# Kernel tuning notes

Hardware: AMD Instinct MI355X
Metric: run time of the kernel (lower is better)

## Reference

```python
import jax, jax.numpy as jnp
import numpy as np

B, T_MEL, CIN = 1, 128, 80
H = 16                      # n_height
N_FLOW, N_LAYER = 8, 8
RES = 128                   # residual = gate = skip = filter_size
IN_CH = 1
T = T_MEL * 256
SQRT_HALF = 0.7071067811865476
DIL_H = [2 ** (i % 3) for i in range(N_LAYER)]
DIL_W = [2 ** i for i in range(N_LAYER)]


def conv1x1(x, w, b):
    # x: [B,C,H,W], w: [O,C], b: [O]
    return jnp.einsum('oc,bchw->bohw', w, x) + b[None, :, None, None]


def causal_conv(x, w, b, dh, dw):
    # 3x3 conv, causal over height (pad top 2*dh), same over width
    out = jax.lax.conv_general_dilated(x, w, (1, 1), ((2 * dh, 0), (dw, dw)),
                                       rhs_dilation=(dh, dw),
                                       dimension_numbers=('NCHW', 'OIHW', 'NCHW'))
    return out + b[None, :, None, None]


def conv_transpose_1ch(x, w, b):
    # torch ConvTranspose2d(1,1,(3,32),padding=(1,8),stride=(1,16)) as dilated conv
    wf = w[::-1, ::-1][None, None]  # flipped kernel [1,1,3,32]
    out = jax.lax.conv_general_dilated(x, wf, (1, 1), ((1, 1), (23, 23)),
                                       lhs_dilation=(1, 16),
                                       dimension_numbers=('NCHW', 'OIHW', 'NCHW'))
    return out + b


def leaky(x):
    return jnp.where(x > 0, x, 0.4 * x)  # LeakyReLU(0.4)


def upsample(c, uw1, ub1, uw2, ub2):
    c = c[:, None]  # [B,1,CIN,T_mel]
    c = leaky(conv_transpose_1ch(c, uw1, ub1))
    c = leaky(conv_transpose_1ch(c, uw2, ub2))
    return c[:, 0]  # [B,CIN,256*T_mel]


def squeeze2d(a, h):
    # [B,C,T] -> [B,C,h,T//h] with adjacent samples along height
    b_, c_, t_ = a.shape
    return a.reshape(b_, c_, t_ // h, h).transpose(0, 1, 3, 2)


def wavenet(x, c, fw, fb, fgw, fgb, fgcw, fgcb, rsw, rsb):
    h = conv1x1(x, fw, fb)  # front 1x1 conv -> RES channels
    skip = 0.0
    for l in range(N_LAYER):
        hg = causal_conv(h, fgw[l], fgb[l], DIL_H[l], DIL_W[l]) + conv1x1(c, fgcw[l], fgcb[l])
        out = jnp.tanh(hg[:, :RES]) * jax.nn.sigmoid(hg[:, RES:])
        h = (h + conv1x1(out, rsw[l], rsb[l])) * SQRT_HALF
        skip = skip + out
    return skip


def waveflow_forward(x, c, front_w, front_b, fg_w, fg_b, fgc_w, fgc_b, rs_w, rs_b,
                     proj_w, proj_b, proj_scale, up_w1, up_b1, up_w2, up_b2):
    c_up = upsample(c, up_w1, up_b1, up_w2, up_b2)[:, :, :T]
    out = squeeze2d(x[:, None], H)   # [B,1,H,W]
    c2 = squeeze2d(c_up, H)          # [B,CIN,H,W]
    logdet = jnp.asarray(0.0, x.dtype)
    for i in range(N_FLOW):
        feat = wavenet(out[:, :, :-1], c2[:, :, 1:],
                       front_w[i], front_b[i], fg_w[i], fg_b[i],
                       fgc_w[i], fgc_b[i], rs_w[i], rs_b[i])
        # ZeroConv2d: 1x1 conv then * exp(3*scale)
        ls_t = conv1x1(feat, proj_w[i], proj_b[i]) * jnp.exp(proj_scale[i] * 3.0)[None, :, None, None]
        log_s, t = ls_t[:, :IN_CH], ls_t[:, IN_CH:]
        x_new = out[:, :, 1:] * jnp.exp(log_s) + t
        out = jnp.concatenate([out[:, :, :1], x_new], axis=2)
        logdet = logdet + jnp.sum(log_s)
        out = out[:, :, ::-1]   # reverse_order over height after every flow
        c2 = c2[:, :, ::-1]
    return out, logdet


def setup_inputs():
    key = jax.random.key(0)
    ks = jax.random.split(key, 10)
    inp = {
        'x': jax.random.normal(ks[0], (B, T), jnp.float32),
        'c': jax.random.normal(ks[1], (B, CIN, T_MEL), jnp.float32),
        'front_w': jax.random.normal(ks[2], (N_FLOW, RES, IN_CH), jnp.float32) * 0.05,
        'front_b': jnp.zeros((N_FLOW, RES), jnp.float32),
        'fg_w': jax.random.normal(ks[3], (N_FLOW, N_LAYER, 2 * RES, RES, 3, 3), jnp.float32) * 0.02,
        'fg_b': jnp.zeros((N_FLOW, N_LAYER, 2 * RES), jnp.float32),
        'fgc_w': jax.random.normal(ks[4], (N_FLOW, N_LAYER, 2 * RES, CIN), jnp.float32) * 0.05,
        'fgc_b': jnp.zeros((N_FLOW, N_LAYER, 2 * RES), jnp.float32),
        'rs_w': jax.random.normal(ks[5], (N_FLOW, N_LAYER, RES, RES), jnp.float32) * 0.05,
        'rs_b': jnp.zeros((N_FLOW, N_LAYER, RES), jnp.float32),
        'proj_w': jax.random.normal(ks[6], (N_FLOW, 2 * IN_CH, RES), jnp.float32) * 0.01,
        'proj_b': jnp.zeros((N_FLOW, 2 * IN_CH), jnp.float32),
        'proj_scale': jnp.zeros((N_FLOW, 2 * IN_CH), jnp.float32),
        'up_w1': jax.random.normal(ks[7], (3, 32), jnp.float32) * 0.1,
        'up_b1': jnp.zeros((), jnp.float32),
        'up_w2': jax.random.normal(ks[8], (3, 32), jnp.float32) * 0.1,
        'up_b2': jnp.zeros((), jnp.float32),
    }
    return inp


def reference(x, c, front_w, front_b, fg_w, fg_b, fgc_w, fgc_b, rs_w, rs_b,
              proj_w, proj_b, proj_scale, up_w1, up_b1, up_w2, up_b2):
    return waveflow_forward(x, c, front_w, front_b, fg_w, fg_b, fgc_w, fgc_b,
                            rs_w, rs_b, proj_w, proj_b, proj_scale,
                            up_w1, up_b1, up_w2, up_b2)
```

## Files before the change

### kernel.cpp

```cpp
#include <hip/hip_runtime.h>
#include <math.h>

#define SQH 0.70710678118654752f
typedef unsigned short u16;
using bf16x8 = __attribute__((ext_vector_type(8))) short;
using f32x4  = __attribute__((ext_vector_type(4))) float;

__device__ __forceinline__ u16 bfhi(float v) {
    unsigned u = __builtin_bit_cast(unsigned, v);
    return (u16)((u + 0x7FFFu + ((u >> 16) & 1u)) >> 16);
}
__device__ __forceinline__ float bf2f(u16 h) {
    unsigned u = ((unsigned)h) << 16;
    return __builtin_bit_cast(float, u);
}
__device__ __forceinline__ void split2(float v, u16& hi, u16& lo) {
    hi = bfhi(v);
    lo = bfhi(v - bf2f(hi));
}
__device__ __forceinline__ void gl_lds16(const void* g, void* l) {
    __builtin_amdgcn_global_load_lds(
        (const __attribute__((address_space(1))) unsigned*)g,
        (__attribute__((address_space(3))) unsigned*)l, 16, 0, 0);
}

__global__ void upsample_k(const float* __restrict__ in, int Tin,
                           const float* __restrict__ w, const float* __restrict__ bb,
                           float* __restrict__ out, int Tout)
{
    int idx = blockIdx.x * 256 + threadIdx.x;
    if (idx >= 80 * Tout) return;
    int oh = idx / Tout, ow = idx - oh * Tout;
    float acc = bb[0];
    int kw0 = (23 - (ow & 15)) & 15;
#pragma unroll
    for (int kh = 0; kh < 3; ++kh) {
        int ih = oh - 1 + kh;
        if (ih < 0 || ih >= 80) continue;
#pragma unroll
        for (int m = 0; m < 2; ++m) {
            int kw = kw0 + 16 * m;
            int j = ow - 23 + kw;
            if (j < 0) continue;
            int src = j >> 4;
            if (src < Tin)
                acc = fmaf(w[(2 - kh) * 32 + (31 - kw)], in[ih * Tin + src], acc);
        }
    }
    out[idx] = acc > 0.f ? acc : 0.4f * acc;
}

__global__ void squeeze_x_k(const float* __restrict__ x, float* __restrict__ o)
{
    int idx = blockIdx.x * 256 + threadIdx.x;
    int i = idx >> 11, j = idx & 2047;
    o[idx] = x[(j << 4) + i];
}

__global__ void zero2_k(float* __restrict__ logdet, float* __restrict__ zbuf)
{
    if (threadIdx.x == 0) logdet[0] = 0.f;
    zbuf[threadIdx.x] = 0.f;
}

__global__ void c2t_k(const float* __restrict__ cup, u16* __restrict__ THi, u16* __restrict__ TLo)
{
    int idx = blockIdx.x * 256 + threadIdx.x;
    int cc = idx % 96; int rt = idx / 96; int t = rt & 2047; int rr = rt >> 11;
    float v = (cc < 80) ? cup[(size_t)cc * 32768 + t * 16 + rr] : 0.f;
    u16 hi, lo; split2(v, hi, lo);
    THi[idx] = hi; TLo[idx] = lo;
}

__global__ void wc_cvt_k(const float* __restrict__ fgw, u16* __restrict__ WHi, u16* __restrict__ WLo)
{
    int idx = blockIdx.x * 256 + threadIdx.x;
    int ic = idx & 127, s = (idx >> 7) & 255, l = idx >> 15;
    int oc = ((s >> 7) << 6) + (((s >> 6) & 1) << 5) + (s & 31) + (((s >> 5) & 1) << 7);
    const float* src = fgw + ((size_t)(l * 256 + oc) * 128 + ic) * 9;
#pragma unroll
    for (int tap = 0; tap < 9; ++tap) {
        u16 hi, lo; split2(src[tap], hi, lo);
        size_t o = ((size_t)(l * 9 + tap) * 256 + s) * 128 + ic;
        WHi[o] = hi; WLo[o] = lo;
    }
}

__global__ void wd_cvt_k(const float* __restrict__ fgcw, u16* __restrict__ WHi, u16* __restrict__ WLo)
{
    int idx = blockIdx.x * 256 + threadIdx.x;
    int cc = idx % 96; int rest = idx / 96; int s = rest & 255; int fl = rest >> 8;
    int oc = ((s >> 7) << 6) + (((s >> 6) & 1) << 5) + (s & 31) + (((s >> 5) & 1) << 7);
    float v = (cc < 80) ? fgcw[((size_t)fl * 256 + oc) * 80 + cc] : 0.f;
    u16 hi, lo; split2(v, hi, lo);
    WHi[idx] = hi; WLo[idx] = lo;
}

__global__ void wrs_cvt_k(const float* __restrict__ rsw, u16* __restrict__ WHi, u16* __restrict__ WLo)
{
    int idx = blockIdx.x * 256 + threadIdx.x;
    u16 hi, lo; split2(rsw[idx], hi, lo);
    WHi[idx] = hi; WLo[idx] = lo;
}

__global__ void front_k(const float* __restrict__ X, float* __restrict__ h,
                        u16* __restrict__ hTHi, u16* __restrict__ hTLo,
                        const float* __restrict__ fw, const float* __restrict__ fb,
                        float* __restrict__ lsacc)
{
    int bid = blockIdx.x, tid = threadIdx.x;
    if (bid < 960) {
        int rt = bid * 32 + (tid >> 3);
        int ch0 = (tid & 7) << 4;
        float xv = X[rt];
        unsigned hs[8], ls[8];
#pragma unroll
        for (int k = 0; k < 16; k += 2) {
            float v0 = fmaf(fw[ch0 + k], xv, fb[ch0 + k]);
            float v1 = fmaf(fw[ch0 + k + 1], xv, fb[ch0 + k + 1]);
            h[(size_t)(ch0 + k) * 30720 + rt] = v0;
            h[(size_t)(ch0 + k + 1) * 30720 + rt] = v1;
            u16 h0, l0, h1, l1; split2(v0, h0, l0); split2(v1, h1, l1);
            hs[k >> 1] = (unsigned)h0 | ((unsigned)h1 << 16);
            ls[k >> 1] = (unsigned)l0 | ((unsigned)l1 << 16);
        }
        uint4* dh4 = (uint4*)(hTHi + (size_t)rt * 128 + ch0);
        dh4[0] = make_uint4(hs[0], hs[1], hs[2], hs[3]);
        dh4[1] = make_uint4(hs[4], hs[5], hs[6], hs[7]);
        uint4* dl4 = (uint4*)(hTLo + (size_t)rt * 128 + ch0);
        dl4[0] = make_uint4(ls[0], ls[1], ls[2], ls[3]);
        dl4[1] = make_uint4(ls[4], ls[5], ls[6], ls[7]);
    } else {
        int i = (bid - 960) * 256 + tid;
        ((float4*)lsacc)[i] = make_float4(0.f, 0.f, 0.f, 0.f);
    }
}

__global__ __launch_bounds__(256)
void conv_gate_mfma(const u16* __restrict__ hTHi, const u16* __restrict__ hTLo,
                    const u16* __restrict__ c2THi, const u16* __restrict__ c2TLo,
                    const u16* __restrict__ WcHi, const u16* __restrict__ WcLo,
                    const u16* __restrict__ WdHi, const u16* __restrict__ WdLo,
                    const float* __restrict__ fgb, const float* __restrict__ fgcb,
                    u16* __restrict__ oTHi, u16* __restrict__ oTLo,
                    const float* __restrict__ zbuf,
                    int dh, int dw, int rev)
{
    __shared__ char lds[32768];
    const int tid = threadIdx.x;
    const int lane = tid & 63, w = tid >> 6;
    const int wm = w & 1, wn = w >> 1;
    const int t0 = blockIdx.x << 7;
    const int r  = blockIdx.y;
    const int ocb = blockIdx.z;
    const int si = lane & 15;
    const int sc = lane >> 4;

    f32x4 acc[4][4];
#pragma unroll
    for (int fm = 0; fm < 4; ++fm) {
        int ocx = (ocb << 6) + (wm << 5) + ((fm & 1) << 4) + ((lane >> 4) << 2) + ((fm >> 1) << 7);
        f32x4 b;
#pragma unroll
        for (int rg = 0; rg < 4; ++rg) b[rg] = fgb[ocx + rg] + fgcb[ocx + rg];
#pragma unroll
        for (int fn = 0; fn < 4; ++fn) acc[fm][fn] = b;
    }

    auto chunk = [&](const u16* aHi, const u16* aLo, int aStr,
                     const u16* bHi, const u16* bLo, int bStr,
                     int k0, int shift, int bounded) {
        __syncthreads();
#pragma unroll
        for (int e = 0; e < 2; ++e) {
            int rowA = (w << 5) + (e << 4) + si;
            int lb = (w << 11) + (e << 10);
            gl_lds16(aHi + (size_t)rowA * aStr + k0 + sc * 8, lds + lb);
            gl_lds16(aLo + (size_t)rowA * aStr + k0 + sc * 8, lds + 8192 + lb);
            int cc = t0 + rowA + shift;
            const u16* sh = bHi + (size_t)cc * bStr + k0 + sc * 8;
            const u16* sl = bLo + (size_t)cc * bStr + k0 + sc * 8;
            if (bounded && (unsigned)cc >= 2048u) { sh = (const u16*)zbuf; sl = (const u16*)zbuf; }
            gl_lds16(sh, lds + 16384 + lb);
            gl_lds16(sl, lds + 24576 + lb);
        }
        __syncthreads();
        bf16x8 aF[4][2];
#pragma unroll
        for (int fm = 0; fm < 4; ++fm) {
            int off = (((wm << 2) + fm) << 10) + ((lane >> 4) << 8) + ((lane & 15) << 4);
            aF[fm][0] = *(const bf16x8*)(lds + off);
            aF[fm][1] = *(const bf16x8*)(lds + 8192 + off);
        }
#pragma unroll
        for (int fn = 0; fn < 4; ++fn) {
            int off = (((wn << 2) + fn) << 10) + ((lane >> 4) << 8) + ((lane & 15) << 4);
            bf16x8 bH = *(const bf16x8*)(lds + 16384 + off);
            bf16x8 bL = *(const bf16x8*)(lds + 24576 + off);
#pragma unroll
            for (int fm = 0; fm < 4; ++fm) {
                acc[fm][fn] = __builtin_amdgcn_mfma_f32_16x16x32_bf16(aF[fm][0], bH, acc[fm][fn], 0, 0, 0);
                acc[fm][fn] = __builtin_amdgcn_mfma_f32_16x16x32_bf16(aF[fm][1], bH, acc[fm][fn], 0, 0, 0);
                acc[fm][fn] = __builtin_amdgcn_mfma_f32_16x16x32_bf16(aF[fm][0], bL, acc[fm][fn], 0, 0, 0);
            }
        }
    };

    for (int tap = 0; tap < 9; ++tap) {
        int kh = tap / 3, kw = tap - kh * 3;
        int rr = r - (2 - kh) * dh;
        if (rr < 0) continue;
        int shift = (kw - 1) * dw;
        const u16* aHi = WcHi + ((size_t)tap * 256 + (size_t)ocb * 128) * 128;
        const u16* aLo = WcLo + ((size_t)tap * 256 + (size_t)ocb * 128) * 128;
        const u16* bHi = hTHi + (size_t)rr * 2048 * 128;
        const u16* bLo = hTLo + (size_t)rr * 2048 * 128;
        for (int icq = 0; icq < 4; ++icq)
            chunk(aHi, aLo, 128, bHi, bLo, 128, icq * 32, shift, 1);
    }
    {
        int rrow = rev ? (14 - r) : (r + 1);
        const u16* aHi = WdHi + (size_t)ocb * 128 * 96;
        const u16* aLo = WdLo + (size_t)ocb * 128 * 96;
        const u16* bHi = c2THi + (size_t)rrow * 2048 * 96;
        const u16* bLo = c2TLo + (size_t)rrow * 2048 * 96;
        for (int ccq = 0; ccq < 3; ++ccq)
            chunk(aHi, aLo, 96, bHi, bLo, 96, ccq * 32, 0, 0);
    }

    float ov[2][4][4];
#pragma unroll
    for (int q = 0; q < 2; ++q)
#pragma unroll
        for (int fn = 0; fn < 4; ++fn)
#pragma unroll
            for (int rg = 0; rg < 4; ++rg) {
                float tv = acc[q][fn][rg], sv = acc[q + 2][fn][rg];
                ov[q][fn][rg] = tanhf(tv) * (1.f / (1.f + expf(-sv)));
            }

#pragma unroll
    for (int pl = 0; pl < 2; ++pl) {
        __syncthreads();
#pragma unroll
        for (int q = 0; q < 2; ++q)
#pragma unroll
            for (int fn = 0; fn < 4; ++fn) {
                int tl = (wn << 6) + (fn << 4) + (lane & 15);
                int p0 = (wm << 5) + (q << 4) + ((lane >> 4) << 2);
                u16 s[4];
#pragma unroll
                for (int rg = 0; rg < 4; ++rg) {
                    float v = ov[q][fn][rg];
                    u16 hi = bfhi(v);
                    s[rg] = pl ? bfhi(v - bf2f(hi)) : hi;
                }
                uint2 val;
                val.x = (unsigned)s[0] | ((unsigned)s[1] << 16);
                val.y = (unsigned)s[2] | ((unsigned)s[3] << 16);
                *(uint2*)(lds + tl * 128 + ((p0 ^ ((tl & 7) << 3)) << 1)) = val;
            }
        __syncthreads();
        u16* dst = pl ? oTLo : oTHi;
#pragma unroll
        for (int e = 0; e < 4; ++e) {
            int tl = (tid >> 3) + (e << 5);
            int pg = tid & 7;
            uint4 v = *(const uint4*)(lds + tl * 128 + ((pg ^ (tl & 7)) << 4));
            *(uint4*)(dst + ((size_t)r * 2048 + t0 + tl) * 128 + (ocb << 6) + (pg << 3)) = v;
        }
    }
}

__global__ __launch_bounds__(256)
void rs_mfma(float* __restrict__ h, const u16* __restrict__ oTHi, const u16* __restrict__ oTLo,
             const u16* __restrict__ WHi, const u16* __restrict__ WLo,
             const float* __restrict__ rsb,
             u16* __restrict__ hTHi, u16* __restrict__ hTLo)
{
    __shared__ char lds[24576];
    const int tid = threadIdx.x;
    const int lane = tid & 63, w = tid >> 6;
    const int wm = w & 1, wn = w >> 1;
    const int t0 = blockIdx.x << 6;
    const int r = blockIdx.y;
    const int si = lane & 15, sc = lane >> 4;

    f32x4 acc[4][2];
#pragma unroll
    for (int fm = 0; fm < 4; ++fm)
#pragma unroll
        for (int fn = 0; fn < 2; ++fn)
#pragma unroll
            for (int rg = 0; rg < 4; ++rg) acc[fm][fn][rg] = 0.f;

    for (int icq = 0; icq < 4; ++icq) {
        int k0 = icq * 32;
        __syncthreads();
#pragma unroll
        for (int e = 0; e < 2; ++e) {
            int rowA = (w << 5) + (e << 4) + si;
            int lb = (w << 11) + (e << 10);
            gl_lds16(WHi + (size_t)rowA * 128 + k0 + sc * 8, lds + lb);
            gl_lds16(WLo + (size_t)rowA * 128 + k0 + sc * 8, lds + 8192 + lb);
        }
        {
            int tt = (w << 4) + si;
            int lb = (w << 10);
            gl_lds16(oTHi + ((size_t)r * 2048 + t0 + tt) * 128 + k0 + sc * 8, lds + 16384 + lb);
            gl_lds16(oTLo + ((size_t)r * 2048 + t0 + tt) * 128 + k0 + sc * 8, lds + 20480 + lb);
        }
        __syncthreads();
        bf16x8 aF[4][2];
#pragma unroll
        for (int fm = 0; fm < 4; ++fm) {
            int off = (((wm << 2) + fm) << 10) + ((lane >> 4) << 8) + ((lane & 15) << 4);
            aF[fm][0] = *(const bf16x8*)(lds + off);
            aF[fm][1] = *(const bf16x8*)(lds + 8192 + off);
        }
#pragma unroll
        for (int fn = 0; fn < 2; ++fn) {
            int off = (((wn << 1) + fn) << 10) + ((lane >> 4) << 8) + ((lane & 15) << 4);
            bf16x8 bH = *(const bf16x8*)(lds + 16384 + off);
            bf16x8 bL = *(const bf16x8*)(lds + 20480 + off);
#pragma unroll
            for (int fm = 0; fm < 4; ++fm) {
                acc[fm][fn] = __builtin_amdgcn_mfma_f32_16x16x32_bf16(aF[fm][0], bH, acc[fm][fn], 0, 0, 0);
                acc[fm][fn] = __builtin_amdgcn_mfma_f32_16x16x32_bf16(aF[fm][1], bH, acc[fm][fn], 0, 0, 0);
                acc[fm][fn] = __builtin_amdgcn_mfma_f32_16x16x32_bf16(aF[fm][0], bL, acc[fm][fn], 0, 0, 0);
            }
        }
    }

    float hv[4][2][4];
#pragma unroll
    for (int fm = 0; fm < 4; ++fm)
#pragma unroll
        for (int fn = 0; fn < 2; ++fn) {
            int t = t0 + (wn << 5) + (fn << 4) + (lane & 15);
#pragma unroll
            for (int rg = 0; rg < 4; ++rg) {
                int ch = (wm << 6) + (fm << 4) + ((lane >> 4) << 2) + rg;
                size_t off = (size_t)ch * 30720 + (size_t)r * 2048 + t;
                float nv = (h[off] + acc[fm][fn][rg] + rsb[ch]) * SQH;
                h[off] = nv;
                hv[fm][fn][rg] = nv;
            }
        }

#pragma unroll
    for (int pl = 0; pl < 2; ++pl) {
        __syncthreads();
#pragma unroll
        for (int fm = 0; fm < 4; ++fm)
#pragma unroll
            for (int fn = 0; fn < 2; ++fn) {
                int tl = (wn << 5) + (fn << 4) + (lane & 15);
                int ch0 = (wm << 6) + (fm << 4) + ((lane >> 4) << 2);
                u16 s[4];
#pragma unroll
                for (int rg = 0; rg < 4; ++rg) {
                    float v = hv[fm][fn][rg];
                    u16 hi = bfhi(v);
                    s[rg] = pl ? bfhi(v - bf2f(hi)) : hi;
                }
                uint2 val;
                val.x = (unsigned)s[0] | ((unsigned)s[1] << 16);
                val.y = (unsigned)s[2] | ((unsigned)s[3] << 16);
                *(uint2*)(lds + tl * 256 + ((ch0 ^ ((tl & 7) << 3)) << 1)) = val;
            }
        __syncthreads();
        u16* dst = pl ? hTLo : hTHi;
#pragma unroll
        for (int e = 0; e < 4; ++e) {
            int tl = (tid >> 4) + (e << 4);
            int chg = tid & 15;
            uint4 v = *(const uint4*)(lds + tl * 256 + ((chg ^ (tl & 7)) << 4));
            *(uint4*)(dst + ((size_t)r * 2048 + t0 + tl) * 128 + (chg << 3)) = v;
        }
    }
}

__global__ void lsadd_k(float* __restrict__ lsacc, const u16* __restrict__ oTHi,
                        const u16* __restrict__ oTLo, const float* __restrict__ pw)
{
    int idx = blockIdx.x * 256 + threadIdx.x;
    const uint4* ph = (const uint4*)(oTHi + (size_t)idx * 128);
    const uint4* pl = (const uint4*)(oTLo + (size_t)idx * 128);
    float a0 = 0.f, a1 = 0.f;
#pragma unroll 4
    for (int g = 0; g < 16; ++g) {
        uint4 vh = ph[g], vl = pl[g];
        const unsigned* uh = &vh.x; const unsigned* ul = &vl.x;
#pragma unroll
        for (int j = 0; j < 4; ++j) {
            int ic = g * 8 + j * 2;
            float v0 = bf2f((u16)(uh[j] & 0xffffu)) + bf2f((u16)(ul[j] & 0xffffu));
            float v1 = bf2f((u16)(uh[j] >> 16)) + bf2f((u16)(ul[j] >> 16));
            a0 = fmaf(pw[ic], v0, a0);       a0 = fmaf(pw[ic + 1], v1, a0);
            a1 = fmaf(pw[128 + ic], v0, a1); a1 = fmaf(pw[128 + ic + 1], v1, a1);
        }
    }
    lsacc[idx] += a0;
    lsacc[30720 + idx] += a1;
}

__global__ void update_k(const float* __restrict__ Xc, float* __restrict__ Xn,
                         const float* __restrict__ lsacc, const float* __restrict__ pb,
                         const float* __restrict__ psc, float* __restrict__ logdet)
{
    int idx = blockIdx.x * 256 + threadIdx.x;
    int rr = idx >> 11, t = idx & 2047;
    float e0 = expf(3.f * psc[0]), e1 = expf(3.f * psc[1]);
    float ls0 = (lsacc[idx] + pb[0]) * e0;
    float ls1 = (lsacc[30720 + idx] + pb[1]) * e1;
    float xn = fmaf(Xc[idx + 2048], expf(ls0), ls1);
    Xn[(14 - rr) * 2048 + t] = xn;
    if (idx < 2048) Xn[15 * 2048 + idx] = Xc[idx];
    float s = ls0;
#pragma unroll
    for (int o = 32; o > 0; o >>= 1) s += __shfl_down(s, o);
    if ((threadIdx.x & 63) == 0) atomicAdd(logdet, s);
}

extern "C" void kernel_launch(void* const* d_in, const int* in_sizes, int n_in,
                              void* d_out, int out_size, void* d_ws, size_t ws_size,
                              hipStream_t stream)
{
    const float* x       = (const float*)d_in[0];
    const float* c       = (const float*)d_in[1];
    const float* front_w = (const float*)d_in[2];
    const float* front_b = (const float*)d_in[3];
    const float* fg_w    = (const float*)d_in[4];
    const float* fg_b    = (const float*)d_in[5];
    const float* fgc_w   = (const float*)d_in[6];
    const float* fgc_b   = (const float*)d_in[7];
    const float* rs_w    = (const float*)d_in[8];
    const float* rs_b    = (const float*)d_in[9];
    const float* proj_w  = (const float*)d_in[10];
    const float* proj_b  = (const float*)d_in[11];
    const float* proj_s  = (const float*)d_in[12];
    const float* up_w1   = (const float*)d_in[13];
    const float* up_b1   = (const float*)d_in[14];
    const float* up_w2   = (const float*)d_in[15];
    const float* up_b2   = (const float*)d_in[16];
    float* out = (float*)d_out;

    float* base = (float*)d_ws;
    float* c1   = base;
    float* cup  = c1 + 163840;
    float* lsac = cup + 2621440;
    float* outA = lsac + 61440;
    float* outB = outA + 32768;
    float* zbuf = outB + 32768;
    float* h    = zbuf + 64;
    u16* u = (u16*)(h + 3932160);
    u16* hTHi = u;  u += 3932160;
    u16* hTLo = u;  u += 3932160;
    u16* oTHi = u;  u += 3932160;
    u16* oTLo = u;  u += 3932160;
    u16* c2THi = u; u += 3145728;
    u16* c2TLo = u; u += 3145728;
    u16* WdHi = u;  u += 1572864;
    u16* WdLo = u;  u += 1572864;
    u16* WrsHi = u; u += 1048576;
    u16* WrsLo = u; u += 1048576;
    u16* WcHi = u;  u += 2359296;
    u16* WcLo = u;  u += 2359296;

    upsample_k<<<640, 256, 0, stream>>>(c, 128, up_w1, up_b1, c1, 2048);
    upsample_k<<<10240, 256, 0, stream>>>(c1, 2048, up_w2, up_b2, cup, 32768);
    c2t_k<<<12288, 256, 0, stream>>>(cup, c2THi, c2TLo);
    squeeze_x_k<<<128, 256, 0, stream>>>(x, outA);
    zero2_k<<<1, 64, 0, stream>>>(out + 32768, zbuf);
    wd_cvt_k<<<6144, 256, 0, stream>>>(fgc_w, WdHi, WdLo);
    wrs_cvt_k<<<4096, 256, 0, stream>>>(rs_w, WrsHi, WrsLo);

    float* Xc = outA;
    float* Xn = outB;
    for (int i = 0; i < 8; ++i) {
        int rev = i & 1;
        wc_cvt_k<<<1024, 256, 0, stream>>>(fg_w + (size_t)i * 2359296, WcHi, WcLo);
        front_k<<<1020, 256, 0, stream>>>(Xc, h, hTHi, hTLo,
                                          front_w + i * 128, front_b + i * 128, lsac);
        for (int l = 0; l < 8; ++l) {
            int fl = i * 8 + l;
            int dh = 1 << (l % 3), dw = 1 << l;
            conv_gate_mfma<<<dim3(16, 15, 2), 256, 0, stream>>>(
                hTHi, hTLo, c2THi, c2TLo,
                WcHi + (size_t)l * 9 * 256 * 128, WcLo + (size_t)l * 9 * 256 * 128,
                WdHi + (size_t)fl * 256 * 96, WdLo + (size_t)fl * 256 * 96,
                fg_b + fl * 256, fgc_b + fl * 256,
                oTHi, oTLo, zbuf, dh, dw, rev);
            lsadd_k<<<120, 256, 0, stream>>>(lsac, oTHi, oTLo, proj_w + i * 256);
            if (l < 7)
                rs_mfma<<<dim3(32, 15), 256, 0, stream>>>(h, oTHi, oTLo,
                    WrsHi + (size_t)fl * 16384, WrsLo + (size_t)fl * 16384,
                    rs_b + fl * 128, hTHi, hTLo);
        }
        float* dst = (i == 7) ? out : Xn;
        update_k<<<120, 256, 0, stream>>>(Xc, dst, lsac, proj_b + i * 2,
                                          proj_s + i * 2, out + 32768);
        float* tmp = Xc; Xc = Xn; Xn = tmp;
    }
}
```

Before: 6.417 ms.

## Double-buffer LDS staging in conv_gate and rs GEMMs; split lsadd across four threads

Both MFMA kernels now stage the next K-chunk into a second LDS buffer while computing on the current one. They use explicit vmcnt waits, raw barriers and raised wave priority around the MFMA block, so global-to-LDS loads overlap with matrix math. The projection-reduction kernel splits each row's 128-channel dot product over four threads with shuffle reduction, giving four times as many threads. Doubling LDS per block may reduce occupancy, and the hand-tuned vmcnt counts must match the number of issued loads.

```diff
diff --git a/kernel.cpp b/kernel.cpp
--- a/kernel.cpp
+++ b/kernel.cpp
@@ -5,6 +5,9 @@
 typedef unsigned short u16;
 using bf16x8 = __attribute__((ext_vector_type(8))) short;
 using f32x4  = __attribute__((ext_vector_type(4))) float;
+
+#define HARD_BARRIER() asm volatile("s_barrier" ::: "memory")
+#define SCHED_PIN()    __builtin_amdgcn_sched_barrier(0)
 
 __device__ __forceinline__ u16 bfhi(float v) {
     unsigned u = __builtin_bit_cast(unsigned, v);
@@ -146,7 +149,7 @@
                     const float* __restrict__ zbuf,
                     int dh, int dw, int rev)
 {
-    __shared__ char lds[32768];
+    __shared__ char lds[65536];
     const int tid = threadIdx.x;
     const int lane = tid & 63, w = tid >> 6;
     const int wm = w & 1, wn = w >> 1;
@@ -156,10 +159,15 @@
     const int si = lane & 15;
     const int sc = lane >> 4;
 
+    const int khmin = (r >= 2 * dh) ? 0 : ((r >= dh) ? 1 : 2);
+    const int nconv = (3 - khmin) * 12;
+    const int n = nconv + 3;
+    const int rrow = rev ? (14 - r) : (r + 1);
+
     f32x4 acc[4][4];
 #pragma unroll
     for (int fm = 0; fm < 4; ++fm) {
-        int ocx = (ocb << 6) + (wm << 5) + ((fm & 1) << 4) + ((lane >> 4) << 2) + ((fm >> 1) << 7);
+        int ocx = (ocb << 6) + (wm << 5) + ((fm & 1) << 4) + (sc << 2) + ((fm >> 1) << 7);
         f32x4 b;
 #pragma unroll
         for (int rg = 0; rg < 4; ++rg) b[rg] = fgb[ocx + rg] + fgcb[ocx + rg];
@@ -167,66 +175,85 @@
         for (int fn = 0; fn < 4; ++fn) acc[fm][fn] = b;
     }
 
-    auto chunk = [&](const u16* aHi, const u16* aLo, int aStr,
-                     const u16* bHi, const u16* bLo, int bStr,
-                     int k0, int shift, int bounded) {
-        __syncthreads();
+    auto STAGE = [&](int ci, char* bufb) {
+        const u16 *aH, *aL, *bH, *bL;
+        int aStr, bStr, k0, shift, bounded;
+        if (ci < nconv) {
+            int tap = khmin * 3 + (ci >> 2);
+            int kh = tap / 3, kw = tap - kh * 3;
+            shift = (kw - 1) * dw;
+            int rr = r - (2 - kh) * dh;
+            size_t aOff = ((size_t)tap * 256 + (size_t)ocb * 128) * 128;
+            aH = WcHi + aOff; aL = WcLo + aOff;
+            size_t bOff = (size_t)rr * 262144;
+            bH = hTHi + bOff; bL = hTLo + bOff;
+            aStr = 128; bStr = 128; k0 = (ci & 3) << 5; bounded = 1;
+        } else {
+            int q = ci - nconv;
+            size_t aOff = (size_t)ocb * 12288;
+            aH = WdHi + aOff; aL = WdLo + aOff;
+            size_t bOff = (size_t)rrow * 196608;
+            bH = c2THi + bOff; bL = c2TLo + bOff;
+            aStr = 96; bStr = 96; k0 = q << 5; shift = 0; bounded = 0;
+        }
 #pragma unroll
         for (int e = 0; e < 2; ++e) {
             int rowA = (w << 5) + (e << 4) + si;
             int lb = (w << 11) + (e << 10);
-            gl_lds16(aHi + (size_t)rowA * aStr + k0 + sc * 8, lds + lb);
-            gl_lds16(aLo + (size_t)rowA * aStr + k0 + sc * 8, lds + 8192 + lb);
+            gl_lds16(aH + (size_t)rowA * aStr + k0 + sc * 8, bufb + lb);
+            gl_lds16(aL + (size_t)rowA * aStr + k0 + sc * 8, bufb + 8192 + lb);
             int cc = t0 + rowA + shift;
-            const u16* sh = bHi + (size_t)cc * bStr + k0 + sc * 8;
-            const u16* sl = bLo + (size_t)cc * bStr + k0 + sc * 8;
+            const u16* sh = bH + (size_t)cc * bStr + k0 + sc * 8;
+            const u16* sl = bL + (size_t)cc * bStr + k0 + sc * 8;
             if (bounded && (unsigned)cc >= 2048u) { sh = (const u16*)zbuf; sl = (const u16*)zbuf; }
-            gl_lds16(sh, lds + 16384 + lb);
-            gl_lds16(sl, lds + 24576 + lb);
-        }
-        __syncthreads();
+            gl_lds16(sh, bufb + 16384 + lb);
+            gl_lds16(sl, bufb + 24576 + lb);
+        }
+    };
+
+    auto COMPUTE = [&](const char* bufb) {
         bf16x8 aF[4][2];
 #pragma unroll
         for (int fm = 0; fm < 4; ++fm) {
-            int off = (((wm << 2) + fm) << 10) + ((lane >> 4) << 8) + ((lane & 15) << 4);
-            aF[fm][0] = *(const bf16x8*)(lds + off);
-            aF[fm][1] = *(const bf16x8*)(lds + 8192 + off);
-        }
+            int off = (((wm << 2) + fm) << 10) + (sc << 8) + (si << 4);
+            aF[fm][0] = *(const bf16x8*)(bufb + off);
+            aF[fm][1] = *(const bf16x8*)(bufb + 8192 + off);
+        }
+        __builtin_amdgcn_s_setprio(1);
 #pragma unroll
         for (int fn = 0; fn < 4; ++fn) {
-            int off = (((wn << 2) + fn) << 10) + ((lane >> 4) << 8) + ((lane & 15) << 4);
-            bf16x8 bH = *(const bf16x8*)(lds + 16384 + off);
-            bf16x8 bL = *(const bf16x8*)(lds + 24576 + off);
+            int off = (((wn << 2) + fn) << 10) + (sc << 8) + (si << 4);
+            bf16x8 bH8 = *(const bf16x8*)(bufb + 16384 + off);
+            bf16x8 bL8 = *(const bf16x8*)(bufb + 24576 + off);
 #pragma unroll
             for (int fm = 0; fm < 4; ++fm) {
-                acc[fm][fn] = __builtin_amdgcn_mfma_f32_16x16x32_bf16(aF[fm][0], bH, acc[fm][fn], 0, 0, 0);
-                acc[fm][fn] = __builtin_amdgcn_mfma_f32_16x16x32_bf16(aF[fm][1], bH, acc[fm][fn], 0, 0, 0);
-                acc[fm][fn] = __builtin_amdgcn_mfma_f32_16x16x32_bf16(aF[fm][0], bL, acc[fm][fn], 0, 0, 0);
+                acc[fm][fn] = __builtin_amdgcn_mfma_f32_16x16x32_bf16(aF[fm][0], bH8, acc[fm][fn], 0, 0, 0);
+                acc[fm][fn] = __builtin_amdgcn_mfma_f32_16x16x32_bf16(aF[fm][1], bH8, acc[fm][fn], 0, 0, 0);
+                acc[fm][fn] = __builtin_amdgcn_mfma_f32_16x16x32_bf16(aF[fm][0], bL8, acc[fm][fn], 0, 0, 0);
             }
         }
+        __builtin_amdgcn_s_setprio(0);
     };
 
-    for (int tap = 0; tap < 9; ++tap) {
-        int kh = tap / 3, kw = tap - kh * 3;
-        int rr = r - (2 - kh) * dh;
-        if (rr < 0) continue;
-        int shift = (kw - 1) * dw;
-        const u16* aHi = WcHi + ((size_t)tap * 256 + (size_t)ocb * 128) * 128;
-        const u16* aLo = WcLo + ((size_t)tap * 256 + (size_t)ocb * 128) * 128;
-        const u16* bHi = hTHi + (size_t)rr * 2048 * 128;
-        const u16* bLo = hTLo + (size_t)rr * 2048 * 128;
-        for (int icq = 0; icq < 4; ++icq)
-            chunk(aHi, aLo, 128, bHi, bLo, 128, icq * 32, shift, 1);
-    }
-    {
-        int rrow = rev ? (14 - r) : (r + 1);
-        const u16* aHi = WdHi + (size_t)ocb * 128 * 96;
-        const u16* aLo = WdLo + (size_t)ocb * 128 * 96;
-        const u16* bHi = c2THi + (size_t)rrow * 2048 * 96;
-        const u16* bLo = c2TLo + (size_t)rrow * 2048 * 96;
-        for (int ccq = 0; ccq < 3; ++ccq)
-            chunk(aHi, aLo, 96, bHi, bLo, 96, ccq * 32, 0, 0);
-    }
+    STAGE(0, lds);
+    int cur = 0;
+    for (int ci = 0; ci < n - 1; ++ci) {
+        STAGE(ci + 1, lds + ((cur ^ 1) << 15));
+        asm volatile("s_waitcnt vmcnt(8)" ::: "memory");
+        SCHED_PIN();
+        HARD_BARRIER();
+        SCHED_PIN();
+        COMPUTE(lds + (cur << 15));
+        SCHED_PIN();
+        HARD_BARRIER();
+        SCHED_PIN();
+        cur ^= 1;
+    }
+    asm volatile("s_waitcnt vmcnt(0)" ::: "memory");
+    SCHED_PIN();
+    HARD_BARRIER();
+    SCHED_PIN();
+    COMPUTE(lds + (cur << 15));
 
     float ov[2][4][4];
 #pragma unroll
@@ -246,8 +273,8 @@
         for (int q = 0; q < 2; ++q)
 #pragma unroll
             for (int fn = 0; fn < 4; ++fn) {
-                int tl = (wn << 6) + (fn << 4) + (lane & 15);
-                int p0 = (wm << 5) + (q << 4) + ((lane >> 4) << 2);
+                int tl = (wn << 6) + (fn << 4) + si;
+                int p0 = (wm << 5) + (q << 4) + (sc << 2);
                 u16 s[4];
 #pragma unroll
                 for (int rg = 0; rg < 4; ++rg) {
@@ -278,7 +305,7 @@
              const float* __restrict__ rsb,
              u16* __restrict__ hTHi, u16* __restrict__ hTLo)
 {
-    __shared__ char lds[24576];
+    __shared__ char lds[49152];
     const int tid = threadIdx.x;
     const int lane = tid & 63, w = tid >> 6;
     const int wm = w & 1, wn = w >> 1;
@@ -294,53 +321,74 @@
 #pragma unroll
             for (int rg = 0; rg < 4; ++rg) acc[fm][fn][rg] = 0.f;
 
-    for (int icq = 0; icq < 4; ++icq) {
-        int k0 = icq * 32;
-        __syncthreads();
+    auto STAGE = [&](int icq, char* bufb) {
+        int k0 = icq << 5;
 #pragma unroll
         for (int e = 0; e < 2; ++e) {
             int rowA = (w << 5) + (e << 4) + si;
             int lb = (w << 11) + (e << 10);
-            gl_lds16(WHi + (size_t)rowA * 128 + k0 + sc * 8, lds + lb);
-            gl_lds16(WLo + (size_t)rowA * 128 + k0 + sc * 8, lds + 8192 + lb);
-        }
-        {
-            int tt = (w << 4) + si;
-            int lb = (w << 10);
-            gl_lds16(oTHi + ((size_t)r * 2048 + t0 + tt) * 128 + k0 + sc * 8, lds + 16384 + lb);
-            gl_lds16(oTLo + ((size_t)r * 2048 + t0 + tt) * 128 + k0 + sc * 8, lds + 20480 + lb);
-        }
-        __syncthreads();
+            gl_lds16(WHi + (size_t)rowA * 128 + k0 + sc * 8, bufb + lb);
+            gl_lds16(WLo + (size_t)rowA * 128 + k0 + sc * 8, bufb + 8192 + lb);
+        }
+        int tt = (w << 4) + si;
+        int lb = (w << 10);
+        gl_lds16(oTHi + ((size_t)r * 2048 + t0 + tt) * 128 + k0 + sc * 8, bufb + 16384 + lb);
+        gl_lds16(oTLo + ((size_t)r * 2048 + t0 + tt) * 128 + k0 + sc * 8, bufb + 20480 + lb);
+    };
+
+    auto COMPUTE = [&](const char* bufb) {
         bf16x8 aF[4][2];
 #pragma unroll
         for (int fm = 0; fm < 4; ++fm) {
-            int off = (((wm << 2) + fm) << 10) + ((lane >> 4) << 8) + ((lane & 15) << 4);
-            aF[fm][0] = *(const bf16x8*)(lds + off);
-            aF[fm][1] = *(const bf16x8*)(lds + 8192 + off);
-        }
+            int off = (((wm << 2) + fm) << 10) + (sc << 8) + (si << 4);
+            aF[fm][0] = *(const bf16x8*)(bufb + off);
+            aF[fm][1] = *(const bf16x8*)(bufb + 8192 + off);
+        }
+        __builtin_amdgcn_s_setprio(1);
 #pragma unroll
         for (int fn = 0; fn < 2; ++fn) {
-            int off = (((wn << 1) + fn) << 10) + ((lane >> 4) << 8) + ((lane & 15) << 4);
-            bf16x8 bH = *(const bf16x8*)(lds + 16384 + off);
-            bf16x8 bL = *(const bf16x8*)(lds + 20480 + off);
+            int off = (((wn << 1) + fn) << 10) + (sc << 8) + (si << 4);
+            bf16x8 bH8 = *(const bf16x8*)(bufb + 16384 + off);
+            bf16x8 bL8 = *(const bf16x8*)(bufb + 20480 + off);
 #pragma unroll
             for (int fm = 0; fm < 4; ++fm) {
-                acc[fm][fn] = __builtin_amdgcn_mfma_f32_16x16x32_bf16(aF[fm][0], bH, acc[fm][fn], 0, 0, 0);
-                acc[fm][fn] = __builtin_amdgcn_mfma_f32_16x16x32_bf16(aF[fm][1], bH, acc[fm][fn], 0, 0, 0);
-                acc[fm][fn] = __builtin_amdgcn_mfma_f32_16x16x32_bf16(aF[fm][0], bL, acc[fm][fn], 0, 0, 0);
+                acc[fm][fn] = __builtin_amdgcn_mfma_f32_16x16x32_bf16(aF[fm][0], bH8, acc[fm][fn], 0, 0, 0);
+                acc[fm][fn] = __builtin_amdgcn_mfma_f32_16x16x32_bf16(aF[fm][1], bH8, acc[fm][fn], 0, 0, 0);
+                acc[fm][fn] = __builtin_amdgcn_mfma_f32_16x16x32_bf16(aF[fm][0], bL8, acc[fm][fn], 0, 0, 0);
             }
         }
-    }
+        __builtin_amdgcn_s_setprio(0);
+    };
+
+    STAGE(0, lds);
+    int cur = 0;
+    for (int icq = 0; icq < 3; ++icq) {
+        STAGE(icq + 1, lds + (cur ^ 1) * 24576);
+        asm volatile("s_waitcnt vmcnt(6)" ::: "memory");
+        SCHED_PIN();
+        HARD_BARRIER();
+        SCHED_PIN();
+        COMPUTE(lds + cur * 24576);
+        SCHED_PIN();
+        HARD_BARRIER();
+        SCHED_PIN();
+        cur ^= 1;
+    }
+    asm volatile("s_waitcnt vmcnt(0)" ::: "memory");
+    SCHED_PIN();
+    HARD_BARRIER();
+    SCHED_PIN();
+    COMPUTE(lds + cur * 24576);
 
     float hv[4][2][4];
 #pragma unroll
     for (int fm = 0; fm < 4; ++fm)
 #pragma unroll
         for (int fn = 0; fn < 2; ++fn) {
-            int t = t0 + (wn << 5) + (fn << 4) + (lane & 15);
+            int t = t0 + (wn << 5) + (fn << 4) + si;
 #pragma unroll
             for (int rg = 0; rg < 4; ++rg) {
-                int ch = (wm << 6) + (fm << 4) + ((lane >> 4) << 2) + rg;
+                int ch = (wm << 6) + (fm << 4) + (sc << 2) + rg;
                 size_t off = (size_t)ch * 30720 + (size_t)r * 2048 + t;
                 float nv = (h[off] + acc[fm][fn][rg] + rsb[ch]) * SQH;
                 h[off] = nv;
@@ -355,8 +403,8 @@
         for (int fm = 0; fm < 4; ++fm)
 #pragma unroll
             for (int fn = 0; fn < 2; ++fn) {
-                int tl = (wn << 5) + (fn << 4) + (lane & 15);
-                int ch0 = (wm << 6) + (fm << 4) + ((lane >> 4) << 2);
+                int tl = (wn << 5) + (fn << 4) + si;
+                int ch0 = (wm << 6) + (fm << 4) + (sc << 2);
                 u16 s[4];
 #pragma unroll
                 for (int rg = 0; rg < 4; ++rg) {
@@ -384,25 +432,30 @@
 __global__ void lsadd_k(float* __restrict__ lsacc, const u16* __restrict__ oTHi,
                         const u16* __restrict__ oTLo, const float* __restrict__ pw)
 {
-    int idx = blockIdx.x * 256 + threadIdx.x;
-    const uint4* ph = (const uint4*)(oTHi + (size_t)idx * 128);
-    const uint4* pl = (const uint4*)(oTLo + (size_t)idx * 128);
+    int gid = blockIdx.x * 256 + threadIdx.x;
+    int idx = gid >> 2, part = gid & 3;
+    const uint4* ph = (const uint4*)(oTHi + (size_t)idx * 128 + part * 32);
+    const uint4* pl = (const uint4*)(oTLo + (size_t)idx * 128 + part * 32);
     float a0 = 0.f, a1 = 0.f;
-#pragma unroll 4
-    for (int g = 0; g < 16; ++g) {
+#pragma unroll
+    for (int g = 0; g < 4; ++g) {
         uint4 vh = ph[g], vl = pl[g];
         const unsigned* uh = &vh.x; const unsigned* ul = &vl.x;
 #pragma unroll
         for (int j = 0; j < 4; ++j) {
-            int ic = g * 8 + j * 2;
+            int ic = part * 32 + g * 8 + j * 2;
             float v0 = bf2f((u16)(uh[j] & 0xffffu)) + bf2f((u16)(ul[j] & 0xffffu));
             float v1 = bf2f((u16)(uh[j] >> 16)) + bf2f((u16)(ul[j] >> 16));
             a0 = fmaf(pw[ic], v0, a0);       a0 = fmaf(pw[ic + 1], v1, a0);
             a1 = fmaf(pw[128 + ic], v0, a1); a1 = fmaf(pw[128 + ic + 1], v1, a1);
         }
     }
-    lsacc[idx] += a0;
-    lsacc[30720 + idx] += a1;
+    a0 += __shfl_xor(a0, 1); a0 += __shfl_xor(a0, 2);
+    a1 += __shfl_xor(a1, 1); a1 += __shfl_xor(a1, 2);
+    if (part == 0) {
+        lsacc[idx] += a0;
+        lsacc[30720 + idx] += a1;
+    }
 }
 
 __global__ void update_k(const float* __restrict__ Xc, float* __restrict__ Xn,
@@ -492,7 +545,7 @@
                 WdHi + (size_t)fl * 256 * 96, WdLo + (size_t)fl * 256 * 96,
                 fg_b + fl * 256, fgc_b + fl * 256,
                 oTHi, oTLo, zbuf, dh, dw, rev);
-            lsadd_k<<<120, 256, 0, stream>>>(lsac, oTHi, oTLo, proj_w + i * 256);
+            lsadd_k<<<480, 256, 0, stream>>>(lsac, oTHi, oTLo, proj_w + i * 256);
             if (l < 7)
                 rs_mfma<<<dim3(32, 15), 256, 0, stream>>>(h, oTHi, oTLo,
                     WrsHi + (size_t)fl * 16384, WrsLo + (size_t)fl * 16384,
```

Result: no change. 6.524 ms (+1.7%).
